# Performance work log

Measured on AMD Instinct MI355X. Metric: run time of the kernel, lower is better.

Reference implementation:

```python
import jax, jax.numpy as jnp
import numpy as np

N_NODES = 200000
N_EDGES = 6400000
IN_DIM = 15      # pfc_input_dim
POS_DIM = 4      # positional_dim
OUT_DIM = 2      # vtx_classes + 1


def setup_inputs() -> dict:
    key = jax.random.key(0)
    k1, k2, k3, k4, k5, k6, k7 = jax.random.split(key, 7)
    x_pfc = jax.random.normal(k1, (N_NODES, IN_DIM), dtype=jnp.float32)
    edge_index = jax.random.randint(k2, (2, N_EDGES), 0, N_NODES, dtype=jnp.int64)
    s_in = 1.0 / np.sqrt(IN_DIM)
    s_pos = 1.0 / np.sqrt(POS_DIM)
    # PointTransformerConv params: lin, lin_src, lin_dst (no bias), pos_nn = Linear(4, 2)
    W_lin = jax.random.uniform(k3, (OUT_DIM, IN_DIM), jnp.float32, -s_in, s_in)
    W_src = jax.random.uniform(k4, (OUT_DIM, IN_DIM), jnp.float32, -s_in, s_in)
    W_dst = jax.random.uniform(k5, (OUT_DIM, IN_DIM), jnp.float32, -s_in, s_in)
    W_pos = jax.random.uniform(k6, (OUT_DIM, POS_DIM), jnp.float32, -s_pos, s_pos)
    b_pos = jax.random.uniform(k7, (OUT_DIM,), jnp.float32, -s_pos, s_pos)
    return {"x_pfc": x_pfc, "edge_index": edge_index, "W_lin": W_lin,
            "W_src": W_src, "W_dst": W_dst, "W_pos": W_pos, "b_pos": b_pos}


def reference(x_pfc, edge_index, W_lin, W_src, W_dst, W_pos, b_pos):
    n = x_pfc.shape[0]
    pos = x_pfc[:, :POS_DIM]
    # original forward calls ptc_only(x, pos, edge_index.flip(0)):
    # source j = edge_index[1], target i = edge_index[0]
    j = edge_index[1]
    i = edge_index[0]
    # node-level linear maps (N x OUT_DIM)
    v = x_pfc @ W_lin.T
    a_src = x_pfc @ W_src.T
    a_dst = x_pfc @ W_dst.T
    # positional MLP on relative positions (E x OUT_DIM)
    delta = (pos[i] - pos[j]) @ W_pos.T + b_pos
    alpha = a_dst[i] - a_src[j] + delta
    # segment softmax over incoming edges of each target node i
    m = jax.ops.segment_max(alpha, i, num_segments=n)  # -inf for empty segments (never indexed)
    e = jnp.exp(alpha - m[i])
    denom = jax.ops.segment_sum(e, i, num_segments=n)
    attn = e / (denom[i] + 1e-16)
    msg = attn * (v[j] + delta)
    return jax.ops.segment_sum(msg, i, num_segments=n)
```

## Files before the change

### kernel.cpp

```cpp
#include <hip/hip_runtime.h>

#define N_NODES 200000
#define N_EDGES 6400000
#define IN_DIM 15
#define POS_DIM 4

#define CSHIFT 9
#define CMASK 511
#define CW 512
#define NCOARSE ((N_NODES + CW - 1) >> CSHIFT)
#define CHUNK 16384
#define NBLK ((N_EDGES + CHUNK - 1) / CHUNK)
#define CAP 17408

typedef unsigned uv4 __attribute__((ext_vector_type(4)));

__global__ void node_prep(const float* __restrict__ x,
                          const float* __restrict__ Wlin,
                          const float* __restrict__ Wsrc,
                          const float* __restrict__ Wdst,
                          const float* __restrict__ Wpos,
                          float2* __restrict__ tabI,
                          float4* __restrict__ tabJ,
                          float2* __restrict__ pvec)
{
    int n = blockIdx.x * blockDim.x + threadIdx.x;
    if (n >= N_NODES) return;
    const float* xp = x + (long)n * IN_DIM;
    float xv[IN_DIM];
#pragma unroll
    for (int k = 0; k < IN_DIM; ++k) xv[k] = xp[k];

    float p0 = 0.f, p1 = 0.f;
#pragma unroll
    for (int k = 0; k < POS_DIM; ++k) {
        p0 += Wpos[k] * xv[k];
        p1 += Wpos[POS_DIM + k] * xv[k];
    }
    float v0 = 0.f, v1 = 0.f, as0 = 0.f, as1 = 0.f, ad0 = 0.f, ad1 = 0.f;
#pragma unroll
    for (int k = 0; k < IN_DIM; ++k) {
        float xk = xv[k];
        v0  += Wlin[k] * xk;           v1  += Wlin[IN_DIM + k] * xk;
        as0 += Wsrc[k] * xk;           as1 += Wsrc[IN_DIM + k] * xk;
        ad0 += Wdst[k] * xk;           ad1 += Wdst[IN_DIM + k] * xk;
    }
    tabI[n] = make_float2(ad0 + p0, ad1 + p1);
    tabJ[n] = make_float4(as0 + p0, as1 + p1, v0 - p0, v1 - p1);
    pvec[n] = make_float2(p0, p1);
}

__global__ void hist_kernel(const int* __restrict__ idx,
                            unsigned* __restrict__ hist)
{
    __shared__ unsigned h[NCOARSE];
    for (int t = threadIdx.x; t < NCOARSE; t += blockDim.x) h[t] = 0u;
    __syncthreads();
    long s0 = (long)blockIdx.x * CHUNK;
    int end = (int)min((long)CHUNK, (long)N_EDGES - s0);
    for (int t = threadIdx.x * 4; t < end; t += 1024) {
        int4 iv = *(const int4*)(idx + s0 + t);
        atomicAdd(&h[iv.x >> CSHIFT], 1u);
        atomicAdd(&h[iv.y >> CSHIFT], 1u);
        atomicAdd(&h[iv.z >> CSHIFT], 1u);
        atomicAdd(&h[iv.w >> CSHIFT], 1u);
    }
    __syncthreads();
    for (int t = threadIdx.x; t < NCOARSE; t += blockDim.x)
        hist[(unsigned)blockIdx.x * NCOARSE + t] = h[t];
}

__global__ void colscan_kernel(unsigned* __restrict__ hist,
                               unsigned* __restrict__ totals)
{
    __shared__ unsigned s[512];
    int k = blockIdx.x;
    int t = threadIdx.x;
    unsigned v = (t < NBLK) ? hist[(unsigned)t * NCOARSE + k] : 0u;
    s[t] = v;
    __syncthreads();
    for (int off = 1; off < 512; off <<= 1) {
        unsigned add = (t >= off) ? s[t - off] : 0u;
        __syncthreads();
        s[t] += add;
        __syncthreads();
    }
    if (t < NBLK) hist[(unsigned)t * NCOARSE + k] = s[t] - v;
    if (t == NBLK - 1) totals[k] = s[t];
}

__global__ void basescan_kernel(const unsigned* __restrict__ totals,
                                unsigned* __restrict__ base)
{
    __shared__ unsigned s[512];
    int t = threadIdx.x;
    unsigned v = (t < NCOARSE) ? ((totals[t] + 3u) & ~3u) : 0u;
    s[t] = v;
    __syncthreads();
    for (int off = 1; off < 512; off <<= 1) {
        unsigned a = (t >= off) ? s[t - off] : 0u;
        __syncthreads();
        s[t] += a;
        __syncthreads();
    }
    if (t < NCOARSE) base[t] = s[t] - v;
}

__global__ void scatter_kernel(const int* __restrict__ idx,
                               const unsigned* __restrict__ hist,
                               const unsigned* __restrict__ base,
                               unsigned* __restrict__ packed)
{
    __shared__ unsigned stage[CHUNK];
    __shared__ unsigned cnt[512];
    __shared__ unsigned sc[512];
    __shared__ unsigned lloc[512];
    __shared__ unsigned gdst[NCOARSE];
    int b = blockIdx.x;
    int t = threadIdx.x;
    long s0 = (long)b * CHUNK;
    int end = (int)min((long)CHUNK, (long)N_EDGES - s0);
    cnt[t] = 0u;
    __syncthreads();
    for (int e = t * 4; e < end; e += 2048) {
        int4 iv = *(const int4*)(idx + s0 + e);
        atomicAdd(&cnt[iv.x >> CSHIFT], 1u);
        atomicAdd(&cnt[iv.y >> CSHIFT], 1u);
        atomicAdd(&cnt[iv.z >> CSHIFT], 1u);
        atomicAdd(&cnt[iv.w >> CSHIFT], 1u);
    }
    __syncthreads();
    sc[t] = cnt[t];
    __syncthreads();
    for (int o = 1; o < 512; o <<= 1) {
        unsigned a = (t >= o) ? sc[t - o] : 0u;
        __syncthreads();
        sc[t] += a;
        __syncthreads();
    }
    {
        unsigned ex = sc[t] - cnt[t];
        lloc[t] = ex;
        cnt[t] = ex;
        if (t < NCOARSE) gdst[t] = base[t] + hist[(unsigned)b * NCOARSE + t];
    }
    __syncthreads();
    for (int e = t * 4; e < end; e += 2048) {
        int4 iv = *(const int4*)(idx + s0 + e);
        int4 jv = *(const int4*)(idx + N_EDGES + s0 + e);
        unsigned r0 = atomicAdd(&cnt[iv.x >> CSHIFT], 1u);
        unsigned r1 = atomicAdd(&cnt[iv.y >> CSHIFT], 1u);
        unsigned r2 = atomicAdd(&cnt[iv.z >> CSHIFT], 1u);
        unsigned r3 = atomicAdd(&cnt[iv.w >> CSHIFT], 1u);
        stage[r0] = ((unsigned)jv.x << CSHIFT) | (unsigned)(iv.x & CMASK);
        stage[r1] = ((unsigned)jv.y << CSHIFT) | (unsigned)(iv.y & CMASK);
        stage[r2] = ((unsigned)jv.z << CSHIFT) | (unsigned)(iv.z & CMASK);
        stage[r3] = ((unsigned)jv.w << CSHIFT) | (unsigned)(iv.w & CMASK);
    }
    __syncthreads();
    int wid = t >> 6, lane = t & 63;
    for (int bk = wid; bk < NCOARSE; bk += 8) {
        unsigned st = lloc[bk];
        unsigned len = ((bk + 1 < 512) ? lloc[bk + 1] : (unsigned)end) - st;
        unsigned gd = gdst[bk];
        for (unsigned e = lane; e < len; e += 64u)
            packed[gd + e] = stage[st + e];
    }
}

__global__ void bucket_agg_kernel(const unsigned* __restrict__ packed,
                                  const unsigned* __restrict__ base,
                                  const unsigned* __restrict__ totals,
                                  const float2* __restrict__ tabI,
                                  const float4* __restrict__ tabJ,
                                  const float2* __restrict__ pvec,
                                  const float* __restrict__ bpos,
                                  float2* __restrict__ out)
{
    __shared__ unsigned cache[CAP + 512];
    __shared__ unsigned cnt[512], sc[512], cur[512];
    int k = blockIdx.x;
    int t = threadIdx.x;
    unsigned s = base[k];
    unsigned n = min(totals[k], (unsigned)CAP);
    cnt[t] = 0u;
    __syncthreads();
    for (unsigned e = 4u * t; e < n; e += 2048u) {
        uv4 p = *(const uv4*)(packed + s + e);
        atomicAdd(&cnt[p.x & CMASK], 1u);
        if (e + 1 < n) atomicAdd(&cnt[p.y & CMASK], 1u);
        if (e + 2 < n) atomicAdd(&cnt[p.z & CMASK], 1u);
        if (e + 3 < n) atomicAdd(&cnt[p.w & CMASK], 1u);
    }
    __syncthreads();
    sc[t] = cnt[t];
    __syncthreads();
    for (int o = 1; o < 512; o <<= 1) {
        unsigned a = (t >= o) ? sc[t - o] : 0u;
        __syncthreads();
        sc[t] += a;
        __syncthreads();
    }
    unsigned deg = cnt[t];
    unsigned st  = sc[t] - deg + (unsigned)t;
    cur[t] = st;
    __syncthreads();
    for (unsigned e = 4u * t; e < n; e += 2048u) {
        uv4 p = __builtin_nontemporal_load((const uv4*)(packed + s + e));
        { unsigned pos = atomicAdd(&cur[p.x & CMASK], 1u); cache[pos] = p.x >> CSHIFT; }
        if (e + 1 < n) { unsigned pos = atomicAdd(&cur[p.y & CMASK], 1u); cache[pos] = p.y >> CSHIFT; }
        if (e + 2 < n) { unsigned pos = atomicAdd(&cur[p.z & CMASK], 1u); cache[pos] = p.z >> CSHIFT; }
        if (e + 3 < n) { unsigned pos = atomicAdd(&cur[p.w & CMASK], 1u); cache[pos] = p.w >> CSHIFT; }
    }
    __syncthreads();
    float b0 = bpos[0], b1 = bpos[1];
    int gn = (k << CSHIFT) + t;
    if (gn >= N_NODES) return;
    float2 fi = tabI[gn];
    float a0 = fi.x + b0, a1 = fi.y + b1;
    float sn0 = 0.f, sn1 = 0.f, sd0 = 0.f, sd1 = 0.f;
    unsigned e = 0;
    for (; e + 4u <= deg; e += 4u) {
        unsigned j0 = cache[st + e],     j1 = cache[st + e + 1];
        unsigned j2 = cache[st + e + 2], j3 = cache[st + e + 3];
        float4 f0 = tabJ[j0], f1 = tabJ[j1], f2 = tabJ[j2], f3 = tabJ[j3];
        float e00 = __expf(a0 - f0.x), e01 = __expf(a1 - f0.y);
        float e10 = __expf(a0 - f1.x), e11 = __expf(a1 - f1.y);
        float e20 = __expf(a0 - f2.x), e21 = __expf(a1 - f2.y);
        float e30 = __expf(a0 - f3.x), e31 = __expf(a1 - f3.y);
        sn0 += e00 * f0.z + e10 * f1.z + e20 * f2.z + e30 * f3.z;
        sn1 += e01 * f0.w + e11 * f1.w + e21 * f2.w + e31 * f3.w;
        sd0 += e00 + e10 + e20 + e30;
        sd1 += e01 + e11 + e21 + e31;
    }
    for (; e < deg; ++e) {
        unsigned j = cache[st + e];
        float4 fj = tabJ[j];
        float e0 = __expf(a0 - fj.x), e1 = __expf(a1 - fj.y);
        sn0 += e0 * fj.z;  sn1 += e1 * fj.w;
        sd0 += e0;         sd1 += e1;
    }
    float2 p = pvec[gn];
    float o0 = (sn0 + (p.x + b0) * sd0) / (sd0 + 1e-16f);
    float o1 = (sn1 + (p.y + b1) * sd1) / (sd1 + 1e-16f);
    out[gn] = make_float2(o0, o1);
}

extern "C" void kernel_launch(void* const* d_in, const int* in_sizes, int n_in,
                              void* d_out, int out_size, void* d_ws, size_t ws_size,
                              hipStream_t stream) {
    const float* x    = (const float*)d_in[0];
    const int*   idx  = (const int*)d_in[1];
    const float* Wlin = (const float*)d_in[2];
    const float* Wsrc = (const float*)d_in[3];
    const float* Wdst = (const float*)d_in[4];
    const float* Wpos = (const float*)d_in[5];
    const float* bpos = (const float*)d_in[6];
    float* out = (float*)d_out;

    char* ws = (char*)d_ws;
    size_t off = 0;
    float4* tabJ = (float4*)(ws + off); off += (size_t)N_NODES * 16;
    float2* tabI = (float2*)(ws + off); off += (size_t)N_NODES * 8;
    float2* pvec = (float2*)(ws + off); off += (size_t)N_NODES * 8;
    unsigned* packed = (unsigned*)(ws + off); off += ((size_t)N_EDGES + 4u * NCOARSE) * 4;
    unsigned* hist   = (unsigned*)(ws + off); off += (size_t)NBLK * NCOARSE * 4;
    unsigned* totals = (unsigned*)(ws + off); off += (size_t)NCOARSE * 4;
    unsigned* base   = (unsigned*)(ws + off); off += (size_t)NCOARSE * 4;

    node_prep<<<(N_NODES + 255) / 256, 256, 0, stream>>>(x, Wlin, Wsrc, Wdst, Wpos,
                                                         tabI, tabJ, pvec);
    hist_kernel<<<NBLK, 256, 0, stream>>>(idx, hist);
    colscan_kernel<<<NCOARSE, 512, 0, stream>>>(hist, totals);
    basescan_kernel<<<1, 512, 0, stream>>>(totals, base);
    scatter_kernel<<<NBLK, 512, 0, stream>>>(idx, hist, base, packed);
    bucket_agg_kernel<<<NCOARSE, 512, 0, stream>>>(packed, base, totals,
                                                   tabI, tabJ, pvec, bpos,
                                                   (float2*)out);
}
```

Before: 178.9 us.

## Halve coarse bucket width and split each node's edges across two threads

Coarse buckets shrink from 512 to 256 nodes, giving about 782 buckets instead of 391. Every scan and count array in the scatter and base-scan kernels grows to 1024 entries to match. In the aggregation kernel, two threads now share each target node, each taking half its incoming edges, and their partial softmax sums are combined with a lane shuffle. The aim is more blocks and twice the parallelism in the gather-heavy aggregation, at the cost of more per-block scan work and extra launch blocks.

```diff
diff --git a/kernel.cpp b/kernel.cpp
--- a/kernel.cpp
+++ b/kernel.cpp
@@ -5,13 +5,13 @@
 #define IN_DIM 15
 #define POS_DIM 4
 
-#define CSHIFT 9
-#define CMASK 511
-#define CW 512
+#define CSHIFT 8
+#define CMASK 255
+#define CW 256
 #define NCOARSE ((N_NODES + CW - 1) >> CSHIFT)
 #define CHUNK 16384
 #define NBLK ((N_EDGES + CHUNK - 1) / CHUNK)
-#define CAP 17408
+#define CAP 9216
 
 typedef unsigned uv4 __attribute__((ext_vector_type(4)));
 
@@ -58,7 +58,7 @@
     __syncthreads();
     long s0 = (long)blockIdx.x * CHUNK;
     int end = (int)min((long)CHUNK, (long)N_EDGES - s0);
-    for (int t = threadIdx.x * 4; t < end; t += 1024) {
+    for (int t = threadIdx.x * 4; t < end; t += 2048) {
         int4 iv = *(const int4*)(idx + s0 + t);
         atomicAdd(&h[iv.x >> CSHIFT], 1u);
         atomicAdd(&h[iv.y >> CSHIFT], 1u);
@@ -92,18 +92,22 @@
 __global__ void basescan_kernel(const unsigned* __restrict__ totals,
                                 unsigned* __restrict__ base)
 {
-    __shared__ unsigned s[512];
+    __shared__ unsigned s[1024];
     int t = threadIdx.x;
-    unsigned v = (t < NCOARSE) ? ((totals[t] + 3u) & ~3u) : 0u;
-    s[t] = v;
-    __syncthreads();
-    for (int off = 1; off < 512; off <<= 1) {
-        unsigned a = (t >= off) ? s[t - off] : 0u;
-        __syncthreads();
-        s[t] += a;
-        __syncthreads();
-    }
-    if (t < NCOARSE) base[t] = s[t] - v;
+    int e0 = t, e1 = t + 512;
+    unsigned v0 = (e0 < NCOARSE) ? ((totals[e0] + 3u) & ~3u) : 0u;
+    unsigned v1 = (e1 < NCOARSE) ? ((totals[e1] + 3u) & ~3u) : 0u;
+    s[e0] = v0; s[e1] = v1;
+    __syncthreads();
+    for (int off = 1; off < 1024; off <<= 1) {
+        unsigned a0 = (e0 >= off) ? s[e0 - off] : 0u;
+        unsigned a1 = (e1 >= off) ? s[e1 - off] : 0u;
+        __syncthreads();
+        s[e0] += a0; s[e1] += a1;
+        __syncthreads();
+    }
+    if (e0 < NCOARSE) base[e0] = s[e0] - v0;
+    if (e1 < NCOARSE) base[e1] = s[e1] - v1;
 }
 
 __global__ void scatter_kernel(const int* __restrict__ idx,
@@ -112,15 +116,15 @@
                                unsigned* __restrict__ packed)
 {
     __shared__ unsigned stage[CHUNK];
-    __shared__ unsigned cnt[512];
-    __shared__ unsigned sc[512];
-    __shared__ unsigned lloc[512];
-    __shared__ unsigned gdst[NCOARSE];
+    __shared__ unsigned cnt[1024];
+    __shared__ unsigned sc[1024];
+    __shared__ unsigned lloc[1025];
+    __shared__ unsigned gdst[1024];
     int b = blockIdx.x;
     int t = threadIdx.x;
     long s0 = (long)b * CHUNK;
     int end = (int)min((long)CHUNK, (long)N_EDGES - s0);
-    cnt[t] = 0u;
+    cnt[t] = 0u; cnt[t + 512] = 0u;
     __syncthreads();
     for (int e = t * 4; e < end; e += 2048) {
         int4 iv = *(const int4*)(idx + s0 + e);
@@ -130,19 +134,24 @@
         atomicAdd(&cnt[iv.w >> CSHIFT], 1u);
     }
     __syncthreads();
-    sc[t] = cnt[t];
-    __syncthreads();
-    for (int o = 1; o < 512; o <<= 1) {
-        unsigned a = (t >= o) ? sc[t - o] : 0u;
-        __syncthreads();
-        sc[t] += a;
+    sc[t] = cnt[t]; sc[t + 512] = cnt[t + 512];
+    __syncthreads();
+    for (int o = 1; o < 1024; o <<= 1) {
+        unsigned a0 = (t >= o) ? sc[t - o] : 0u;
+        unsigned a1 = (t + 512 >= o) ? sc[t + 512 - o] : 0u;
+        __syncthreads();
+        sc[t] += a0; sc[t + 512] += a1;
         __syncthreads();
     }
     {
-        unsigned ex = sc[t] - cnt[t];
-        lloc[t] = ex;
-        cnt[t] = ex;
+        unsigned ex0 = sc[t] - cnt[t];
+        unsigned ex1 = sc[t + 512] - cnt[t + 512];
+        lloc[t] = ex0; lloc[t + 512] = ex1;
+        cnt[t] = ex0; cnt[t + 512] = ex1;
         if (t < NCOARSE) gdst[t] = base[t] + hist[(unsigned)b * NCOARSE + t];
+        int u = t + 512;
+        if (u < NCOARSE) gdst[u] = base[u] + hist[(unsigned)b * NCOARSE + u];
+        if (t == 0) lloc[1024] = (unsigned)end;
     }
     __syncthreads();
     for (int e = t * 4; e < end; e += 2048) {
@@ -159,9 +168,10 @@
     }
     __syncthreads();
     int wid = t >> 6, lane = t & 63;
-    for (int bk = wid; bk < NCOARSE; bk += 8) {
+    for (int bk = wid; bk < 1024; bk += 8) {
         unsigned st = lloc[bk];
-        unsigned len = ((bk + 1 < 512) ? lloc[bk + 1] : (unsigned)end) - st;
+        unsigned len = lloc[bk + 1] - st;
+        if (len == 0u) continue;
         unsigned gd = gdst[bk];
         for (unsigned e = lane; e < len; e += 64u)
             packed[gd + e] = stage[st + e];
@@ -177,13 +187,13 @@
                                   const float* __restrict__ bpos,
                                   float2* __restrict__ out)
 {
-    __shared__ unsigned cache[CAP + 512];
-    __shared__ unsigned cnt[512], sc[512], cur[512];
+    __shared__ unsigned cache[CAP + 256];
+    __shared__ unsigned cnt[256], sc[256], cur[256];
     int k = blockIdx.x;
     int t = threadIdx.x;
     unsigned s = base[k];
     unsigned n = min(totals[k], (unsigned)CAP);
-    cnt[t] = 0u;
+    if (t < 256) cnt[t] = 0u;
     __syncthreads();
     for (unsigned e = 4u * t; e < n; e += 2048u) {
         uv4 p = *(const uv4*)(packed + s + e);
@@ -193,17 +203,16 @@
         if (e + 3 < n) atomicAdd(&cnt[p.w & CMASK], 1u);
     }
     __syncthreads();
-    sc[t] = cnt[t];
-    __syncthreads();
-    for (int o = 1; o < 512; o <<= 1) {
-        unsigned a = (t >= o) ? sc[t - o] : 0u;
-        __syncthreads();
-        sc[t] += a;
-        __syncthreads();
-    }
-    unsigned deg = cnt[t];
-    unsigned st  = sc[t] - deg + (unsigned)t;
-    cur[t] = st;
+    if (t < 256) sc[t] = cnt[t];
+    __syncthreads();
+    for (int o = 1; o < 256; o <<= 1) {
+        unsigned a = 0u;
+        if (t < 256 && t >= o) a = sc[t - o];
+        __syncthreads();
+        if (t < 256) sc[t] += a;
+        __syncthreads();
+    }
+    if (t < 256) cur[t] = sc[t] - cnt[t] + (unsigned)t;
     __syncthreads();
     for (unsigned e = 4u * t; e < n; e += 2048u) {
         uv4 p = __builtin_nontemporal_load((const uv4*)(packed + s + e));
@@ -213,14 +222,19 @@
         if (e + 3 < n) { unsigned pos = atomicAdd(&cur[p.w & CMASK], 1u); cache[pos] = p.w >> CSHIFT; }
     }
     __syncthreads();
+    int m = t >> 1, q = t & 1;
+    int gn = (k << CSHIFT) + m;
+    if (gn >= N_NODES) return;
+    unsigned deg = cnt[m];
+    unsigned st  = sc[m] - deg + (unsigned)m;
+    unsigned h   = (deg >> 1) & ~3u;
+    unsigned lo  = q ? h : 0u, hi = q ? deg : h;
     float b0 = bpos[0], b1 = bpos[1];
-    int gn = (k << CSHIFT) + t;
-    if (gn >= N_NODES) return;
     float2 fi = tabI[gn];
     float a0 = fi.x + b0, a1 = fi.y + b1;
     float sn0 = 0.f, sn1 = 0.f, sd0 = 0.f, sd1 = 0.f;
-    unsigned e = 0;
-    for (; e + 4u <= deg; e += 4u) {
+    unsigned e = lo;
+    for (; e + 4u <= hi; e += 4u) {
         unsigned j0 = cache[st + e],     j1 = cache[st + e + 1];
         unsigned j2 = cache[st + e + 2], j3 = cache[st + e + 3];
         float4 f0 = tabJ[j0], f1 = tabJ[j1], f2 = tabJ[j2], f3 = tabJ[j3];
@@ -233,17 +247,23 @@
         sd0 += e00 + e10 + e20 + e30;
         sd1 += e01 + e11 + e21 + e31;
     }
-    for (; e < deg; ++e) {
+    for (; e < hi; ++e) {
         unsigned j = cache[st + e];
         float4 fj = tabJ[j];
         float e0 = __expf(a0 - fj.x), e1 = __expf(a1 - fj.y);
         sn0 += e0 * fj.z;  sn1 += e1 * fj.w;
         sd0 += e0;         sd1 += e1;
     }
-    float2 p = pvec[gn];
-    float o0 = (sn0 + (p.x + b0) * sd0) / (sd0 + 1e-16f);
-    float o1 = (sn1 + (p.y + b1) * sd1) / (sd1 + 1e-16f);
-    out[gn] = make_float2(o0, o1);
+    sn0 += __shfl_xor(sn0, 1);
+    sn1 += __shfl_xor(sn1, 1);
+    sd0 += __shfl_xor(sd0, 1);
+    sd1 += __shfl_xor(sd1, 1);
+    if (q == 0) {
+        float2 p = pvec[gn];
+        float o0 = (sn0 + (p.x + b0) * sd0) / (sd0 + 1e-16f);
+        float o1 = (sn1 + (p.y + b1) * sd1) / (sd1 + 1e-16f);
+        out[gn] = make_float2(o0, o1);
+    }
 }
 
 extern "C" void kernel_launch(void* const* d_in, const int* in_sizes, int n_in,
@@ -270,7 +290,7 @@
 
     node_prep<<<(N_NODES + 255) / 256, 256, 0, stream>>>(x, Wlin, Wsrc, Wdst, Wpos,
                                                          tabI, tabJ, pvec);
-    hist_kernel<<<NBLK, 256, 0, stream>>>(idx, hist);
+    hist_kernel<<<NBLK, 512, 0, stream>>>(idx, hist);
     colscan_kernel<<<NCOARSE, 512, 0, stream>>>(hist, totals);
     basescan_kernel<<<1, 512, 0, stream>>>(totals, base);
     scatter_kernel<<<NBLK, 512, 0, stream>>>(idx, hist, base, packed);
```

New measurement: 211.8 us. 1.18x slower.
